# Optimization experiments

Measured on AMD Instinct MI355X. Metric: run time of the kernel, lower is better.

Reference implementation:

```python
import jax, jax.numpy as jnp
import numpy as np

B, MBS, F, CD = 512, 32768, 512, 16  # batch, mini_batch_size, filter_length, cond_dim

def setup_inputs() -> dict:
    key = jax.random.key(0)
    ks = jax.random.split(key, 8)
    return {
        "inputs": jax.random.normal(ks[0], (B, MBS, 1), jnp.float32),
        "c": jax.random.normal(ks[1], (B, 1, CD), jnp.float32),
        "W0": jax.random.normal(ks[2], (CD, F), jnp.float32) * 0.1,
        "b0": jnp.zeros((F,), jnp.float32),
        "alpha": jnp.full((F,), 0.25, jnp.float32),
        "Wg": jax.random.normal(ks[3], (CD, F), jnp.float32) * 0.1,
        "bg": jnp.zeros((F,), jnp.float32),
        "Wb": jax.random.normal(ks[4], (CD, F), jnp.float32) * 0.1,
        "bb": jnp.zeros((F,), jnp.float32),
        "Wglu": jax.random.normal(ks[5], (F, 2 * F), jnp.float32) * 0.05,
        "bglu": jnp.zeros((2 * F,), jnp.float32),
        "Wf": jax.random.normal(ks[6], (F, F), jnp.float32) * 0.05,
        "bf": jnp.zeros((F,), jnp.float32),
    }

def reference(inputs, c, W0, b0, alpha, Wg, bg, Wb, bb, Wglu, bglu, Wf, bf):
    mbs = inputs.shape[1]
    flen = Wf.shape[1]
    # conditioning stack: Dense -> PReLU -> FiLM -> GLU -> Dense(softsign)
    c_ = c @ W0 + b0                                  # [B,1,F]
    c_ = jnp.where(c_ >= 0, c_, alpha * c_)           # PReLU
    c_ = c_ * (c @ Wg + bg) + (c @ Wb + bb)           # FiLM
    g = c_ @ Wglu + bglu                              # [B,1,2F]
    a, gate = jnp.split(g, 2, axis=-1)
    c_ = a * jax.nn.sigmoid(gate)                     # GLU
    filters = jax.nn.soft_sign(c_ @ Wf + bf)          # [B,1,F]
    # FFT-based circular (linear via zero pad) convolution
    conv_len = mbs + flen - 1
    X = jnp.fft.fft(inputs[:, :, 0].astype(jnp.complex64), n=conv_len)   # [B,conv_len]
    H = jnp.fft.fft(filters[:, 0, :].astype(jnp.complex64), n=conv_len)  # [B,conv_len]
    y = jnp.fft.ifft(X * H)
    return jnp.real(y[:, :mbs])                       # [B,MBS]
```

## Files before the change

### kernel.cpp

```cpp
#include <hip/hip_runtime.h>


typedef float f32x16 __attribute__((ext_vector_type(16)));
typedef float f32x4  __attribute__((ext_vector_type(4)));
typedef __bf16 bf16x8 __attribute__((ext_vector_type(8)));

__device__ __forceinline__ unsigned short f2bf(float f) {
    unsigned int u = __float_as_uint(f);
    u += 0x7FFFu + ((u >> 16) & 1u);
    return (unsigned short)(u >> 16);
}

__device__ __forceinline__ uint4 pack8n(float4 a, float4 b) {
    bf16x8 v;
    v[0] = (__bf16)a.x; v[1] = (__bf16)a.y; v[2] = (__bf16)a.z; v[3] = (__bf16)a.w;
    v[4] = (__bf16)b.x; v[5] = (__bf16)b.y; v[6] = (__bf16)b.z; v[7] = (__bf16)b.w;
    uint4 r;
    __builtin_memcpy(&r, &v, 16);
    return r;
}

__global__ __launch_bounds__(256) void kA(
    const float* __restrict__ Wglu, const float* __restrict__ Wf,
    const float* __restrict__ c, const float* __restrict__ W0,
    const float* __restrict__ b0, const float* __restrict__ alpha,
    const float* __restrict__ Wg, const float* __restrict__ bg,
    const float* __restrict__ Wb, const float* __restrict__ bb,
    unsigned short* __restrict__ WgluT, unsigned short* __restrict__ WfT,
    unsigned short* __restrict__ cfilm) {
    const int blk = blockIdx.x, tid = threadIdx.x;
    if (blk < 192) {
        __shared__ float ldsF[64 * 65];
        const float* src; unsigned short* dst; int tj, tk, srcld;
        if (blk < 128) { tj = blk >> 3; tk = blk & 7; src = Wglu; dst = WgluT; srcld = 1024; }
        else { int b2 = blk - 128; tj = b2 >> 3; tk = b2 & 7; src = Wf; dst = WfT; srcld = 512; }
#pragma unroll
        for (int rr = 0; rr < 16; ++rr) {
            int kl = (tid >> 6) + (rr << 2), jl = tid & 63;
            ldsF[kl * 65 + jl] = src[(size_t)(tk * 64 + kl) * srcld + tj * 64 + jl];
        }
        __syncthreads();
#pragma unroll
        for (int rr = 0; rr < 16; ++rr) {
            int jl = (tid >> 6) + (rr << 2), kl = tid & 63;
            dst[(size_t)(tj * 64 + jl) * 512 + tk * 64 + kl] = f2bf(ldsF[kl * 65 + jl]);
        }
    } else {
        int id = (blk - 192) * 256 + tid;
        int b = id >> 9, f = id & 511;
        const float* cb = c + b * 16;
        float d0 = 0.f, dg = 0.f, db = 0.f;
#pragma unroll
        for (int i = 0; i < 16; ++i) {
            float cv = cb[i];
            d0 += cv * W0[i * 512 + f];
            dg += cv * Wg[i * 512 + f];
            db += cv * Wb[i * 512 + f];
        }
        float pre = d0 + b0[f];
        float pr = pre >= 0.f ? pre : alpha[f] * pre;
        float v = pr * (dg + bg[f]) + (db + bb[f]);
        cfilm[id] = f2bf(v);
    }
}

__global__ __launch_bounds__(256) void k2_glu(
    const unsigned short* __restrict__ cfilm, const unsigned short* __restrict__ WgluT,
    const float* __restrict__ bglu, unsigned short* __restrict__ cglu) {
    int wid = (blockIdx.x * 256 + threadIdx.x) >> 6;
    int l = threadIdx.x & 63;
    int tm = wid >> 5, tn = wid & 31;
    int row = tm * 16 + (l & 15);
    int col = tn * 16 + (l & 15);
    int kh = 8 * (l >> 4);
    f32x4 accA, accG;
#pragma unroll
    for (int i = 0; i < 4; ++i) { accA[i] = 0.f; accG[i] = 0.f; }
    const unsigned short* ap  = cfilm + row * 512 + kh;
    const unsigned short* bap = WgluT + col * 512 + kh;
    const unsigned short* bgp = WgluT + (512 + col) * 512 + kh;
#pragma unroll
    for (int kc = 0; kc < 16; ++kc) {
        bf16x8 a   = *(const bf16x8*)(ap  + kc * 32);
        bf16x8 ba  = *(const bf16x8*)(bap + kc * 32);
        bf16x8 bgt = *(const bf16x8*)(bgp + kc * 32);
        accA = __builtin_amdgcn_mfma_f32_16x16x32_bf16(a, ba,  accA, 0, 0, 0);
        accG = __builtin_amdgcn_mfma_f32_16x16x32_bf16(a, bgt, accG, 0, 0, 0);
    }
    float biasA = bglu[col], biasG = bglu[512 + col];
#pragma unroll
    for (int r = 0; r < 4; ++r) {
        float ga = accA[r] + biasA;
        float gg = accG[r] + biasG;
        float s = 1.f / (1.f + expf(-gg));
        int m = (l >> 4) * 4 + r;
        cglu[(tm * 16 + m) * 512 + col] = f2bf(ga * s);
    }
}

__global__ __launch_bounds__(256) void k3_filt(
    const unsigned short* __restrict__ cglu, const unsigned short* __restrict__ WfT,
    const float* __restrict__ bfv, unsigned short* __restrict__ hout) {
    int wid = (blockIdx.x * 256 + threadIdx.x) >> 6;
    int l = threadIdx.x & 63;
    int tm = wid >> 5, tn = wid & 31;
    int row = tm * 16 + (l & 15);
    int col = tn * 16 + (l & 15);
    int kh = 8 * (l >> 4);
    f32x4 acc;
#pragma unroll
    for (int i = 0; i < 4; ++i) acc[i] = 0.f;
    const unsigned short* ap = cglu + row * 512 + kh;
    const unsigned short* bp = WfT + col * 512 + kh;
#pragma unroll
    for (int kc = 0; kc < 16; ++kc) {
        bf16x8 a  = *(const bf16x8*)(ap + kc * 32);
        bf16x8 bv = *(const bf16x8*)(bp + kc * 32);
        acc = __builtin_amdgcn_mfma_f32_16x16x32_bf16(a, bv, acc, 0, 0, 0);
    }
    float bias = bfv[col];
#pragma unroll
    for (int r = 0; r < 4; ++r) {
        float z = acc[r] + bias;
        float h = z / (1.f + fabsf(z));
        int m = (l >> 4) * 4 + r;
        hout[(tm * 16 + m) * 512 + col] = f2bf(h);
    }
}

__global__ __launch_bounds__(256, 5) void k7(
    const float* __restrict__ x, const unsigned short* __restrict__ hbf,
    float* __restrict__ y) {
    __shared__ __align__(16) unsigned char smem[27776];
    const int tid = threadIdx.x;
    const int nb = blockIdx.x;
    const int virt = ((nb >> 5) << 5) + ((nb & 7) << 2) + ((nb >> 3) & 3);
    const int b = virt >> 2;
    const int n0 = (virt & 3) << 13;
    const float* xb = x + (size_t)b * 32768;
    unsigned short* hs = (unsigned short*)(smem + 26752);

    ((unsigned int*)hs)[tid] = ((const unsigned int*)(hbf + (size_t)b * 512))[tid];
    __syncthreads();

    for (int e = tid; e < 8 * 292; e += 256) {
        int s = e / 292, w = e - s * 292;
        int j0 = 2 * w + s;
        unsigned int v0 = (j0 >= 32 && j0 < 544) ? hs[543 - j0] : 0u;
        unsigned int v1 = (j0 >= 31 && j0 < 543) ? hs[542 - j0] : 0u;
        ((unsigned int*)(smem + 17408))[e] = v0 | (v1 << 16);
    }

#pragma unroll
    for (int r2 = 0; r2 < 5; ++r2) {
        int slot = tid + (r2 << 8);
        if (slot < 1088) {
            int off = n0 + ((slot - 64) << 3);
            uint4 w4;
            if (off >= 0) {
                float4 a  = *(const float4*)(xb + off);
                float4 b2 = *(const float4*)(xb + off + 4);
                w4 = pack8n(a, b2);
            } else {
                w4 = make_uint4(0u, 0u, 0u, 0u);
            }
            *(uint4*)(smem + ((slot ^ ((slot >> 3) & 7)) << 4)) = w4;
        }
    }
    __syncthreads();

    const int w = tid >> 6, l = tid & 63;
    const int q = l & 31, hl = l >> 5;
    const int lq = 4 * q + hl;
    const int abase = 66 + (w << 8) + lq;
    const int o0 = 559 - q + 8 * hl;
    const int s8 = o0 & 7;
    const unsigned char* hrb = smem + 17408 + s8 * 1168 + ((o0 - s8) << 1);

    f32x16 acc0, acc1;
#pragma unroll
    for (int i = 0; i < 16; ++i) { acc0[i] = 0.f; acc1[i] = 0.f; }
#pragma unroll
    for (int cc = 0; cc < 34; ++cc) {
        bf16x8 bfr = *(const bf16x8*)(hrb - (cc << 5));
        int a0 = abase - 2 * cc, a1 = a0 + 128;
        bf16x8 xa0 = *(const bf16x8*)(smem + ((a0 ^ ((a0 >> 3) & 7)) << 4));
        bf16x8 xa1 = *(const bf16x8*)(smem + ((a1 ^ ((a1 >> 3) & 7)) << 4));
        acc0 = __builtin_amdgcn_mfma_f32_32x32x16_bf16(xa0, bfr, acc0, 0, 0, 0);
        acc1 = __builtin_amdgcn_mfma_f32_32x32x16_bf16(xa1, bfr, acc1, 0, 0, 0);
    }
    float* yb = y + (size_t)b * 32768 + n0 + (w << 11) + q;
#pragma unroll
    for (int r = 0; r < 16; ++r) {
        int m = (r & 3) + 8 * (r >> 2) + 4 * hl;
        yb[m << 5] = acc0[r];
        yb[1024 + (m << 5)] = acc1[r];
    }
}

extern "C" void kernel_launch(void* const* d_in, const int* in_sizes, int n_in,
                              void* d_out, int out_size, void* d_ws, size_t ws_size,
                              hipStream_t stream) {
    const float* x    = (const float*)d_in[0];
    const float* c    = (const float*)d_in[1];
    const float* W0   = (const float*)d_in[2];
    const float* b0   = (const float*)d_in[3];
    const float* al   = (const float*)d_in[4];
    const float* Wg   = (const float*)d_in[5];
    const float* bg   = (const float*)d_in[6];
    const float* Wb   = (const float*)d_in[7];
    const float* bb   = (const float*)d_in[8];
    const float* Wglu = (const float*)d_in[9];
    const float* bglu = (const float*)d_in[10];
    const float* Wf   = (const float*)d_in[11];
    const float* bf   = (const float*)d_in[12];
    float* y = (float*)d_out;

    char* ws = (char*)d_ws;
    unsigned short* cfilm = (unsigned short*)(ws);
    unsigned short* WgluT = (unsigned short*)(ws + 524288);
    unsigned short* WfT   = (unsigned short*)(ws + 1572864);
    unsigned short* cglu  = (unsigned short*)(ws + 2097152);
    unsigned short* hbf   = (unsigned short*)(ws + 2621440);

    kA<<<dim3(1216), dim3(256), 0, stream>>>(Wglu, Wf, c, W0, b0, al, Wg, bg, Wb, bb,
                                             WgluT, WfT, cfilm);
    k2_glu<<<dim3(256), dim3(256), 0, stream>>>(cfilm, WgluT, bglu, cglu);
    k3_filt<<<dim3(256), dim3(256), 0, stream>>>(cglu, WfT, bf, hbf);
    k7<<<dim3(2048), dim3(256), 0, stream>>>(x, hbf, y);
}
```

Before: 52.88 us.

## Double the work per block and prefetch the next input chunk during MFMA compute

The convolution kernel now launches half as many blocks, each covering 16384 outputs. Every wave owns a private input staging buffer and handles two 2048-output chunks. The global loads for the second chunk are issued into registers before the first chunk's MFMA loop and written to LDS after it, so load latency overlaps compute and the block-level barrier before the second chunk is dropped. In exchange it uses more registers and LDS (occupancy hint lowered from 5 to 4) and launches fewer blocks, and the earlier block-index swizzle is removed.

After: 60.01 us. 13.5% more time.

```diff
diff --git a/kernel.cpp b/kernel.cpp
--- a/kernel.cpp
+++ b/kernel.cpp
@@ -128,73 +128,102 @@
     }
 }
 
-__global__ __launch_bounds__(256, 5) void k7(
+__global__ __launch_bounds__(256, 4) void k8(
     const float* __restrict__ x, const unsigned short* __restrict__ hbf,
     float* __restrict__ y) {
-    __shared__ __align__(16) unsigned char smem[27776];
+    __shared__ __align__(16) unsigned char smem[30848];
     const int tid = threadIdx.x;
-    const int nb = blockIdx.x;
-    const int virt = ((nb >> 5) << 5) + ((nb & 7) << 2) + ((nb >> 3) & 3);
-    const int b = virt >> 2;
-    const int n0 = (virt & 3) << 13;
+    const int b = blockIdx.x >> 1;
+    const int n0 = (blockIdx.x & 1) << 14;
     const float* xb = x + (size_t)b * 32768;
-    unsigned short* hs = (unsigned short*)(smem + 26752);
+    unsigned short* hs = (unsigned short*)(smem + 29824);
 
     ((unsigned int*)hs)[tid] = ((const unsigned int*)(hbf + (size_t)b * 512))[tid];
     __syncthreads();
 
     for (int e = tid; e < 8 * 292; e += 256) {
-        int s = e / 292, w = e - s * 292;
-        int j0 = 2 * w + s;
+        int s = e / 292, wv = e - s * 292;
+        int j0 = 2 * wv + s;
         unsigned int v0 = (j0 >= 32 && j0 < 544) ? hs[543 - j0] : 0u;
         unsigned int v1 = (j0 >= 31 && j0 < 543) ? hs[542 - j0] : 0u;
-        ((unsigned int*)(smem + 17408))[e] = v0 | (v1 << 16);
-    }
-
-#pragma unroll
-    for (int r2 = 0; r2 < 5; ++r2) {
-        int slot = tid + (r2 << 8);
-        if (slot < 1088) {
-            int off = n0 + ((slot - 64) << 3);
-            uint4 w4;
-            if (off >= 0) {
-                float4 a  = *(const float4*)(xb + off);
-                float4 b2 = *(const float4*)(xb + off + 4);
-                w4 = pack8n(a, b2);
-            } else {
-                w4 = make_uint4(0u, 0u, 0u, 0u);
-            }
-            *(uint4*)(smem + ((slot ^ ((slot >> 3) & 7)) << 4)) = w4;
-        }
+        ((unsigned int*)(smem + 20480))[e] = v0 | (v1 << 16);
     }
     __syncthreads();
 
     const int w = tid >> 6, l = tid & 63;
     const int q = l & 31, hl = l >> 5;
-    const int lq = 4 * q + hl;
-    const int abase = 66 + (w << 8) + lq;
+    unsigned char* mybuf = smem + w * 5120;
     const int o0 = 559 - q + 8 * hl;
     const int s8 = o0 & 7;
-    const unsigned char* hrb = smem + 17408 + s8 * 1168 + ((o0 - s8) << 1);
-
-    f32x16 acc0, acc1;
-#pragma unroll
-    for (int i = 0; i < 16; ++i) { acc0[i] = 0.f; acc1[i] = 0.f; }
-#pragma unroll
-    for (int cc = 0; cc < 34; ++cc) {
-        bf16x8 bfr = *(const bf16x8*)(hrb - (cc << 5));
-        int a0 = abase - 2 * cc, a1 = a0 + 128;
-        bf16x8 xa0 = *(const bf16x8*)(smem + ((a0 ^ ((a0 >> 3) & 7)) << 4));
-        bf16x8 xa1 = *(const bf16x8*)(smem + ((a1 ^ ((a1 >> 3) & 7)) << 4));
-        acc0 = __builtin_amdgcn_mfma_f32_32x32x16_bf16(xa0, bfr, acc0, 0, 0, 0);
-        acc1 = __builtin_amdgcn_mfma_f32_32x32x16_bf16(xa1, bfr, acc1, 0, 0, 0);
-    }
-    float* yb = y + (size_t)b * 32768 + n0 + (w << 11) + q;
-#pragma unroll
-    for (int r = 0; r < 16; ++r) {
-        int m = (r & 3) + 8 * (r >> 2) + 4 * hl;
-        yb[m << 5] = acc0[r];
-        yb[1024 + (m << 5)] = acc1[r];
+    const unsigned char* hrb = smem + 20480 + s8 * 1168 + ((o0 - s8) << 1);
+    const int abase = 66 + 4 * q + hl;
+    const int wout = n0 + (w << 12);
+
+#pragma unroll
+    for (int j = 0; j < 5; ++j) {
+        int u = l + (j << 6);
+        int off = wout - 512 + (u << 3);
+        uint4 w4;
+        if (off >= 0) {
+            float4 a  = *(const float4*)(xb + off);
+            float4 b2 = *(const float4*)(xb + off + 4);
+            w4 = pack8n(a, b2);
+        } else {
+            w4 = make_uint4(0u, 0u, 0u, 0u);
+        }
+        *(uint4*)(mybuf + ((u ^ ((u >> 3) & 7)) << 4)) = w4;
+    }
+    asm volatile("s_waitcnt lgkmcnt(0)" ::: "memory");
+    __builtin_amdgcn_sched_barrier(0);
+
+#pragma unroll
+    for (int c = 0; c < 2; ++c) {
+        float4 La0, Lb0, La1, Lb1, La2, Lb2, La3, Lb3, La4, Lb4;
+        if (c == 0) {
+            const float* px = xb + wout + 1536;
+            La0 = *(const float4*)(px + (l << 3));             Lb0 = *(const float4*)(px + (l << 3) + 4);
+            La1 = *(const float4*)(px + ((l + 64) << 3));      Lb1 = *(const float4*)(px + ((l + 64) << 3) + 4);
+            La2 = *(const float4*)(px + ((l + 128) << 3));     Lb2 = *(const float4*)(px + ((l + 128) << 3) + 4);
+            La3 = *(const float4*)(px + ((l + 192) << 3));     Lb3 = *(const float4*)(px + ((l + 192) << 3) + 4);
+            La4 = *(const float4*)(px + ((l + 256) << 3));     Lb4 = *(const float4*)(px + ((l + 256) << 3) + 4);
+        }
+        f32x16 acc0, acc1;
+#pragma unroll
+        for (int i = 0; i < 16; ++i) { acc0[i] = 0.f; acc1[i] = 0.f; }
+#pragma unroll
+        for (int cc = 0; cc < 34; ++cc) {
+            bf16x8 bfr = *(const bf16x8*)(hrb - (cc << 5));
+            int u0 = abase - 2 * cc, u1 = u0 + 128;
+            bf16x8 xa0 = *(const bf16x8*)(mybuf + ((u0 ^ ((u0 >> 3) & 7)) << 4));
+            bf16x8 xa1 = *(const bf16x8*)(mybuf + ((u1 ^ ((u1 >> 3) & 7)) << 4));
+            acc0 = __builtin_amdgcn_mfma_f32_32x32x16_bf16(xa0, bfr, acc0, 0, 0, 0);
+            acc1 = __builtin_amdgcn_mfma_f32_32x32x16_bf16(xa1, bfr, acc1, 0, 0, 0);
+        }
+        if (c == 0) {
+            asm volatile("s_waitcnt lgkmcnt(0)" ::: "memory");
+            __builtin_amdgcn_sched_barrier(0);
+            {
+                int u = l;
+                *(uint4*)(mybuf + ((u ^ ((u >> 3) & 7)) << 4)) = pack8n(La0, Lb0);
+                u = l + 64;
+                *(uint4*)(mybuf + ((u ^ ((u >> 3) & 7)) << 4)) = pack8n(La1, Lb1);
+                u = l + 128;
+                *(uint4*)(mybuf + ((u ^ ((u >> 3) & 7)) << 4)) = pack8n(La2, Lb2);
+                u = l + 192;
+                *(uint4*)(mybuf + ((u ^ ((u >> 3) & 7)) << 4)) = pack8n(La3, Lb3);
+                u = l + 256;
+                *(uint4*)(mybuf + ((u ^ ((u >> 3) & 7)) << 4)) = pack8n(La4, Lb4);
+            }
+            asm volatile("s_waitcnt lgkmcnt(0)" ::: "memory");
+            __builtin_amdgcn_sched_barrier(0);
+        }
+        float* yb = y + (size_t)b * 32768 + wout + (c << 11) + q;
+#pragma unroll
+        for (int r = 0; r < 16; ++r) {
+            int m = (r & 3) + 8 * (r >> 2) + 4 * hl;
+            yb[m << 5] = acc0[r];
+            yb[1024 + (m << 5)] = acc1[r];
+        }
     }
 }
 
@@ -227,5 +256,5 @@
                                              WgluT, WfT, cfilm);
     k2_glu<<<dim3(256), dim3(256), 0, stream>>>(cfilm, WgluT, bglu, cglu);
     k3_filt<<<dim3(256), dim3(256), 0, stream>>>(cglu, WfT, bf, hbf);
-    k7<<<dim3(2048), dim3(256), 0, stream>>>(x, hbf, y);
-}
+    k8<<<dim3(1024), dim3(256), 0, stream>>>(x, hbf, y);
+}
```
